# Kernel optimization log

Measured on AMD Instinct MI355X. Metric: run time of the kernel, lower is better.

## Reference

```python
import jax, jax.numpy as jnp
import numpy as np

D_MODEL, N_HEADS, D_HEAD = 1024, 16, 64
BATCH, SEQ = 4, 2048


def setup_inputs() -> dict:
    key = jax.random.key(0)
    ks = jax.random.split(key, 10)
    s = 1.0 / np.sqrt(D_MODEL)
    x = jax.random.normal(ks[0], (BATCH, SEQ, D_MODEL), dtype=jnp.float32)
    attention_mask = jax.random.randint(ks[1], (BATCH, SEQ), 0, 2).astype(jnp.bool_)
    # guarantee at least one attended key per batch row (avoid all -inf softmax)
    attention_mask = attention_mask.at[:, 0].set(True)
    def lin(k):
        kw, kb = jax.random.split(k)
        W = jax.random.uniform(kw, (D_MODEL, D_MODEL), jnp.float32, -s, s)
        b = jax.random.uniform(kb, (D_MODEL,), jnp.float32, -s, s)
        return W, b
    Wq, bq = lin(ks[2]); Wk, bk = lin(ks[3]); Wv, bv = lin(ks[4]); Wo, bo = lin(ks[5])
    return {"x": x, "attention_mask": attention_mask,
            "Wq": Wq, "bq": bq, "Wk": Wk, "bk": bk,
            "Wv": Wv, "bv": bv, "Wo": Wo, "bo": bo}


def reference(x, attention_mask, Wq, bq, Wk, bk, Wv, bv, Wo, bo):
    B, S, _ = x.shape
    def proj(W, b):  # [B,S,d_model] -> [B,S,H,Dh]
        return (x @ W + b).reshape(B, S, N_HEADS, D_HEAD)
    q = proj(Wq, bq)
    k = proj(Wk, bk)
    v = proj(Wv, bv)
    scores = jnp.einsum('bqhd,bkhd->bhqk', q, k)  # [B,H,S,S]
    add_mask = jnp.where(attention_mask, 0.0, jnp.inf)[:, None, None, :]
    # faithful order: subtract mask, THEN scale (inf survives division)
    probs = jax.nn.softmax((scores - add_mask) / jnp.sqrt(jnp.float32(D_HEAD)), axis=-1)
    attn = jnp.einsum('bhqk,bkhd->bqhd', probs, v).reshape(B, S, N_HEADS * D_HEAD)
    return attn @ Wo + bo
```

## Files before the change

### kernel.cpp

```cpp
#include <hip/hip_runtime.h>
#include <hip/hip_bf16.h>
#include <math.h>

#define BATCH 4
#define SEQ   2048
#define DM    1024
#define NH    16
#define DH    64
#define MROWS (BATCH * SEQ)

typedef unsigned short ushort_t;
typedef unsigned int   uint_t;
typedef __attribute__((ext_vector_type(8))) short  short8;
typedef __attribute__((ext_vector_type(4))) float  float4v;

#define QSCALE 0.1803368801111244f

__device__ __forceinline__ ushort_t f2bf(float v) {
    uint_t u = __float_as_uint(v);
    u += 0x7FFFu + ((u >> 16) & 1u);
    return (ushort_t)(u >> 16);
}
__device__ __forceinline__ float bf2f(ushort_t h) {
    return __uint_as_float(((uint_t)h) << 16);
}
__device__ __forceinline__ void gload_lds16(const ushort_t* g, ushort_t* lds) {
    __builtin_amdgcn_global_load_lds(
        (const __attribute__((address_space(1))) void*)g,
        (__attribute__((address_space(3))) void*)lds, 16, 0, 0);
}

__global__ __launch_bounds__(256) void conv_x(
    const float* __restrict__ src, ushort_t* __restrict__ dst, int n4)
{
    int i = blockIdx.x * 256 + threadIdx.x;
    if (i >= n4) return;
    float4 v = ((const float4*)src)[i];
    ((ushort4*)dst)[i] = make_ushort4(f2bf(v.x), f2bf(v.y), f2bf(v.z), f2bf(v.w));
}

__global__ __launch_bounds__(256) void convT_w4(
    const float* __restrict__ W0, const float* __restrict__ W1,
    const float* __restrict__ W2, const float* __restrict__ W3,
    ushort_t* __restrict__ fused, ushort_t* __restrict__ woh,
    ushort_t* __restrict__ wol)
{
    __shared__ float sT[64][65];
    const int z = blockIdx.z;
    const float* W = (z == 0) ? W0 : (z == 1) ? W1 : (z == 2) ? W2 : W3;
    ushort_t* ht = (z < 3) ? fused + (size_t)z * 1024 * 1024 : woh;
    const int n0 = blockIdx.x * 64, k0 = blockIdx.y * 64;
    const int t = threadIdx.x;
#pragma unroll
    for (int i = 0; i < 16; i++) {
        int idx = t + i * 256, r = idx >> 6, c = idx & 63;
        sT[r][c] = W[(size_t)(k0 + r) * 1024 + n0 + c];
    }
    __syncthreads();
#pragma unroll
    for (int i = 0; i < 16; i++) {
        int idx = t + i * 256, r = idx >> 6, c = idx & 63;
        float v = sT[c][r];
        ushort_t h = f2bf(v);
        ht[(size_t)(n0 + r) * 1024 + k0 + c] = h;
        if (z == 3) wol[(size_t)(n0 + r) * 1024 + k0 + c] = f2bf(v - bf2f(h));
    }
}

__global__ __launch_bounds__(256) void gemm_qkv(
    const ushort_t* __restrict__ A, const ushort_t* __restrict__ Bt,
    const float* __restrict__ bq, const float* __restrict__ bk,
    const float* __restrict__ bv,
    ushort_t* __restrict__ Qh, ushort_t* __restrict__ Kh,
    ushort_t* __restrict__ Vt)
{
    __shared__ __align__(16) ushort_t smem[8192];
    const int t = threadIdx.x, lane = t & 63, w = t >> 6;
    const int n0 = blockIdx.x * 128, m0 = blockIdx.y * 128;
    const int wm = (w >> 1) * 64, wn = (w & 1) * 64;
    const int lq = lane >> 4, lc = lane & 15;
    const int gl = (lane & 3) ^ ((lane >> 3) & 3);
    const int irow = lane >> 2;
    const int sect = n0 >> 10;
    const float* bsel = (sect == 0) ? bq : (sect == 1) ? bk : bv;
    const float scl = (sect == 0) ? QSCALE : 1.0f;

    float4v acc[4][4];
#pragma unroll
    for (int i = 0; i < 4; i++)
#pragma unroll
        for (int j = 0; j < 4; j++) acc[i][j] = (float4v)(0.0f);

    for (int k0 = 0; k0 < 1024; k0 += 32) {
        __syncthreads();
#pragma unroll
        for (int j = 0; j < 4; j++) {
            const int i = w * 4 + j;
            const ushort_t* src = (i < 8)
                ? A  + (size_t)(m0 + i * 16 + irow) * 1024 + k0 + gl * 8
                : Bt + (size_t)(n0 + (i - 8) * 16 + irow) * 1024 + k0 + gl * 8;
            gload_lds16(src, &smem[i * 512]);
        }
        __syncthreads();

        short8 av[4], bvf[4];
#pragma unroll
        for (int mt = 0; mt < 4; mt++) {
            const int r = wm + mt * 16 + lc;
            av[mt] = *(const short8*)&smem[r * 32 + ((lq ^ ((r >> 1) & 3)) * 8)];
        }
#pragma unroll
        for (int nt = 0; nt < 4; nt++) {
            const int r = wn + nt * 16 + lc;
            bvf[nt] = *(const short8*)&smem[4096 + r * 32 + ((lq ^ ((r >> 1) & 3)) * 8)];
        }
#pragma unroll
        for (int nt = 0; nt < 4; nt++)
#pragma unroll
            for (int mt = 0; mt < 4; mt++)
                acc[mt][nt] = __builtin_amdgcn_mfma_f32_16x16x32_bf16(av[mt], bvf[nt], acc[mt][nt], 0, 0, 0);
    }

#pragma unroll
    for (int nt = 0; nt < 4; nt++) {
        const int nn = (n0 + wn + nt * 16 + lc) & 1023;
        const float bvv = bsel[nn];
        const int h = nn >> 6, d = nn & 63;
#pragma unroll
        for (int mt = 0; mt < 4; mt++) {
            const int mbase = m0 + wm + mt * 16 + lq * 4;
            const int b = mbase >> 11, s0 = mbase & 2047;
            if (sect == 2) {
                ushort_t hh[4];
#pragma unroll
                for (int r = 0; r < 4; r++) hh[r] = f2bf(acc[mt][nt][r] + bvv);
                *(ushort4*)&Vt[((size_t)(b * 16 + h) * 64 + d) * 2048 + s0] =
                    make_ushort4(hh[0], hh[1], hh[2], hh[3]);
            } else {
                ushort_t* dst = (sect == 0) ? Qh : Kh;
#pragma unroll
                for (int r = 0; r < 4; r++)
                    dst[((size_t)(b * 16 + h) * 2048 + s0 + r) * 64 + d] =
                        f2bf((acc[mt][nt][r] + bvv) * scl);
            }
        }
    }
}

__global__ __launch_bounds__(256) void gemm_split3(
    const ushort_t* __restrict__ Ah, const ushort_t* __restrict__ Al,
    const ushort_t* __restrict__ Bh, const ushort_t* __restrict__ Bl,
    const float* __restrict__ bias, float* __restrict__ out)
{
    __shared__ __align__(16) ushort_t smem[16384];
    const int t = threadIdx.x, lane = t & 63, w = t >> 6;
    const int n0 = blockIdx.x * 128, m0 = blockIdx.y * 128;
    const int wm = (w >> 1) * 64, wn = (w & 1) * 64;
    const int lq = lane >> 4, lc = lane & 15;
    const int gl = (lane & 3) ^ ((lane >> 3) & 3);
    const int irow = lane >> 2;

    float4v acc[4][4];
#pragma unroll
    for (int i = 0; i < 4; i++)
#pragma unroll
        for (int j = 0; j < 4; j++) acc[i][j] = (float4v)(0.0f);

    const ushort_t* plane = (w == 0) ? Ah : (w == 1) ? Al : (w == 2) ? Bh : Bl;
    const size_t prow = (size_t)(((w < 2) ? m0 : n0) + irow) * 1024 + gl * 8;

    for (int k0 = 0; k0 < 1024; k0 += 32) {
        __syncthreads();
#pragma unroll
        for (int j = 0; j < 8; j++)
            gload_lds16(plane + prow + (size_t)j * 16384 + k0, &smem[w * 4096 + j * 512]);
        __syncthreads();

        short8 ah[4], al[4];
#pragma unroll
        for (int mt = 0; mt < 4; mt++) {
            const int r = wm + mt * 16 + lc;
            const int off = r * 32 + ((lq ^ ((r >> 1) & 3)) * 8);
            ah[mt] = *(const short8*)&smem[off];
            al[mt] = *(const short8*)&smem[4096 + off];
        }
#pragma unroll
        for (int nt = 0; nt < 4; nt++) {
            const int r = wn + nt * 16 + lc;
            const int off = r * 32 + ((lq ^ ((r >> 1) & 3)) * 8);
            short8 bh = *(const short8*)&smem[8192 + off];
            short8 bl = *(const short8*)&smem[12288 + off];
#pragma unroll
            for (int mt = 0; mt < 4; mt++) {
                acc[mt][nt] = __builtin_amdgcn_mfma_f32_16x16x32_bf16(ah[mt], bh, acc[mt][nt], 0, 0, 0);
                acc[mt][nt] = __builtin_amdgcn_mfma_f32_16x16x32_bf16(al[mt], bh, acc[mt][nt], 0, 0, 0);
                acc[mt][nt] = __builtin_amdgcn_mfma_f32_16x16x32_bf16(ah[mt], bl, acc[mt][nt], 0, 0, 0);
            }
        }
    }

#pragma unroll
    for (int nt = 0; nt < 4; nt++) {
        const int n = n0 + wn + nt * 16 + lc;
        const float bvv = bias[n];
#pragma unroll
        for (int mt = 0; mt < 4; mt++)
#pragma unroll
            for (int r = 0; r < 4; r++) {
                const int m = m0 + wm + mt * 16 + lq * 4 + r;
                out[(size_t)m * 1024 + n] = acc[mt][nt][r] + bvv;
            }
    }
}

__global__ __launch_bounds__(256, 4) void flash_mfma(
    const ushort_t* __restrict__ Q, const ushort_t* __restrict__ K,
    const ushort_t* __restrict__ Vt, const int* __restrict__ mask,
    ushort_t* __restrict__ Oh, ushort_t* __restrict__ Ol)
{
    __shared__ __align__(16) ushort_t smem[18432];
    const int t = threadIdx.x, lane = t & 63, w = t >> 6;
    const int q0 = blockIdx.x * 128;
    const int bh = blockIdx.y, b = bh >> 4, h = bh & 15;
    const int lq = lane >> 4, lc = lane & 15;
    const int wm = w * 32;
    const int gl = (lane & 7) ^ ((lane >> 3) & 7);

    const short8 onesf = (short8)(lc == 0 ? (short)0x3F80 : (short)0);

    {
        const ushort_t NEG = f2bf(-1e30f);
        const int4* mrow = (const int4*)(mask + b * SEQ);
        int4 a = mrow[t * 2], c = mrow[t * 2 + 1];
        ((ushort4*)&smem[16384])[t * 2] =
            make_ushort4(a.x ? 0 : NEG, a.y ? 0 : NEG, a.z ? 0 : NEG, a.w ? 0 : NEG);
        ((ushort4*)&smem[16384])[t * 2 + 1] =
            make_ushort4(c.x ? 0 : NEG, c.y ? 0 : NEG, c.z ? 0 : NEG, c.w ? 0 : NEG);
    }
#pragma unroll
    for (int j = 0; j < 4; j++) {
        const int i = w * 4 + j;
        gload_lds16(Q + ((size_t)bh * SEQ + q0 + i * 8 + (lane >> 3)) * 64 + gl * 8,
                    &smem[i * 512]);
    }
    __syncthreads();

    short8 aq[2][2];
#pragma unroll
    for (int mt = 0; mt < 2; mt++)
#pragma unroll
        for (int kk = 0; kk < 2; kk++) {
            const int r = wm + mt * 16 + lc;
            aq[mt][kk] = *(const short8*)&smem[r * 64 + (((kk * 4 + lq) ^ (r & 7)) * 8)];
        }

    float4v O[2][4];
    float4v lacc[2];
#pragma unroll
    for (int mt = 0; mt < 2; mt++) {
#pragma unroll
        for (int nt = 0; nt < 4; nt++) O[mt][nt] = (float4v)(0.0f);
        lacc[mt] = (float4v)(0.0f);
    }

    for (int kt = 0; kt < 32; kt++) {
        const int k0 = kt * 64;
        __syncthreads();
#pragma unroll
        for (int j = 0; j < 4; j++) {
            const int i = w * 4 + j;
            if (i < 8)
                gload_lds16(K + ((size_t)bh * SEQ + k0 + i * 8 + (lane >> 3)) * 64 + gl * 8,
                            &smem[8192 + i * 512]);
            else
                gload_lds16(Vt + ((size_t)bh * 64 + (i - 8) * 8 + (lane >> 3)) * SEQ + k0 + gl * 8,
                            &smem[12288 + (i - 8) * 512]);
        }
        __syncthreads();

        float4v binit[4];
#pragma unroll
        for (int kt4 = 0; kt4 < 4; kt4++) {
            const ushort4 bb = *(const ushort4*)&smem[16384 + k0 + kt4 * 16 + lq * 4];
            binit[kt4][0] = bf2f(bb.x); binit[kt4][1] = bf2f(bb.y);
            binit[kt4][2] = bf2f(bb.z); binit[kt4][3] = bf2f(bb.w);
        }

        float4v sc[4][2];
#pragma unroll
        for (int kt4 = 0; kt4 < 4; kt4++)
#pragma unroll
            for (int mt = 0; mt < 2; mt++) sc[kt4][mt] = binit[kt4];
#pragma unroll
        for (int kk = 0; kk < 2; kk++) {
#pragma unroll
            for (int kt4 = 0; kt4 < 4; kt4++) {
                const int kr = kt4 * 16 + lc;
                short8 ak = *(const short8*)&smem[8192 + kr * 64 + (((kk * 4 + lq) ^ (kr & 7)) * 8)];
#pragma unroll
                for (int mt = 0; mt < 2; mt++)
                    sc[kt4][mt] = __builtin_amdgcn_mfma_f32_16x16x32_bf16(ak, aq[mt][kk], sc[kt4][mt], 0, 0, 0);
            }
        }

#pragma unroll
        for (int kt4 = 0; kt4 < 4; kt4++) {
#pragma unroll
            for (int mt = 0; mt < 2; mt++) {
                const int qr = wm + mt * 16 + lc;
                const float p0 = __builtin_amdgcn_exp2f(sc[kt4][mt][0]);
                const float p1 = __builtin_amdgcn_exp2f(sc[kt4][mt][1]);
                const float p2 = __builtin_amdgcn_exp2f(sc[kt4][mt][2]);
                const float p3 = __builtin_amdgcn_exp2f(sc[kt4][mt][3]);
                __hip_bfloat162 pk01 = __float22bfloat162_rn(make_float2(p0, p1));
                __hip_bfloat162 pk23 = __float22bfloat162_rn(make_float2(p2, p3));
                *(uint2*)&smem[qr * 64 + (((kt4 * 2 + (lq >> 1)) ^ (qr & 7)) * 8) + (lq & 1) * 4] =
                    make_uint2(*(const uint_t*)&pk01, *(const uint_t*)&pk23);
            }
        }

#pragma unroll
        for (int kk = 0; kk < 2; kk++) {
            short8 ap[2];
#pragma unroll
            for (int mt = 0; mt < 2; mt++) {
                const int qr = wm + mt * 16 + lc;
                ap[mt] = *(const short8*)&smem[qr * 64 + (((kk * 4 + lq) ^ (qr & 7)) * 8)];
            }
#pragma unroll
            for (int mt = 0; mt < 2; mt++)
                lacc[mt] = __builtin_amdgcn_mfma_f32_16x16x32_bf16(ap[mt], onesf, lacc[mt], 0, 0, 0);
#pragma unroll
            for (int nt = 0; nt < 4; nt++) {
                const int d = nt * 16 + lc;
                short8 bv = *(const short8*)&smem[12288 + d * 64 + (((kk * 4 + lq) ^ (d & 7)) * 8)];
#pragma unroll
                for (int mt = 0; mt < 2; mt++)
                    O[mt][nt] = __builtin_amdgcn_mfma_f32_16x16x32_bf16(ap[mt], bv, O[mt][nt], 0, 0, 0);
            }
        }
    }

#pragma unroll
    for (int mt = 0; mt < 2; mt++) {
#pragma unroll
        for (int r = 0; r < 4; r++) {
            const float lsum = __shfl(lacc[mt][r], lane & 48);
            const float inv = 1.0f / lsum;
            const int srow = q0 + wm + mt * 16 + lq * 4 + r;
#pragma unroll
            for (int nt = 0; nt < 4; nt++) {
                const float v = O[mt][nt][r] * inv;
                const ushort_t hh = f2bf(v);
                const size_t idx = ((size_t)(b * SEQ + srow)) * 1024 + h * 64 + nt * 16 + lc;
                Oh[idx] = hh;
                Ol[idx] = f2bf(v - bf2f(hh));
            }
        }
    }
}

extern "C" void kernel_launch(void* const* d_in, const int* in_sizes, int n_in,
                              void* d_out, int out_size, void* d_ws, size_t ws_size,
                              hipStream_t stream) {
    const float* x    = (const float*)d_in[0];
    const int*   mask = (const int*)d_in[1];
    const float* Wq   = (const float*)d_in[2];
    const float* bq   = (const float*)d_in[3];
    const float* Wk   = (const float*)d_in[4];
    const float* bk   = (const float*)d_in[5];
    const float* Wv   = (const float*)d_in[6];
    const float* bv   = (const float*)d_in[7];
    const float* Wo   = (const float*)d_in[8];
    const float* bo   = (const float*)d_in[9];
    float* out = (float*)d_out;

    ushort_t* p = (ushort_t*)d_ws;
    const size_t PLANE  = (size_t)MROWS * DM;
    const size_t WPLANE = (size_t)DM * DM;
    ushort_t* xh  = p;  p += PLANE;
    ushort_t* wf  = p;  p += 3 * WPLANE;
    ushort_t* woh = p;  p += WPLANE;
    ushort_t* wol = p;  p += WPLANE;
    ushort_t* Qh  = p;  p += PLANE;
    ushort_t* Kh  = p;  p += PLANE;
    ushort_t* Vth = p;  p += PLANE;
    ushort_t* Ath = p;  p += PLANE;
    ushort_t* Atl = p;  p += PLANE;

    dim3 blk(256);
    hipLaunchKernelGGL(conv_x, dim3(8192), blk, 0, stream, x, xh, 2097152);
    hipLaunchKernelGGL(convT_w4, dim3(16, 16, 4), blk, 0, stream,
                       Wq, Wk, Wv, Wo, wf, woh, wol);
    hipLaunchKernelGGL(gemm_qkv, dim3(24, 64), blk, 0, stream,
                       xh, wf, bq, bk, bv, Qh, Kh, Vth);
    hipLaunchKernelGGL(flash_mfma, dim3(16, 64), blk, 0, stream,
                       Qh, Kh, Vth, mask, Ath, Atl);
    hipLaunchKernelGGL(gemm_split3, dim3(8, 64), blk, 0, stream,
                       Ath, Atl, woh, wol, bo, out);
}
```

Measured before the change: 326.0 us.

## Fold key mask into K/V projection and correct softmax denominator by masked count

The QKV GEMM epilogue now zeroes K and V rows at masked key positions. Each masked score then becomes exactly 0, giving exp2(0)=1 in the row sum, and the flash kernel subtracts the per-batch masked-key count from the denominator. This removes the per-tile mask-bias load and bf16-to-float conversion from the attention inner loop and shrinks LDS usage. Alongside that, LDS and global addresses are precomputed outside the loop so the tile loads use one strided pointer per wave. The denominator subtraction runs in fp32 against a sum of bf16-rounded probabilities, so cancellation error can appear when most keys are masked.

```diff
diff --git a/kernel.cpp b/kernel.cpp
--- a/kernel.cpp
+++ b/kernel.cpp
@@ -70,7 +70,7 @@
 __global__ __launch_bounds__(256) void gemm_qkv(
     const ushort_t* __restrict__ A, const ushort_t* __restrict__ Bt,
     const float* __restrict__ bq, const float* __restrict__ bk,
-    const float* __restrict__ bv,
+    const float* __restrict__ bv, const int* __restrict__ mask,
     ushort_t* __restrict__ Qh, ushort_t* __restrict__ Kh,
     ushort_t* __restrict__ Vt)
 {
@@ -130,10 +130,16 @@
         for (int mt = 0; mt < 4; mt++) {
             const int mbase = m0 + wm + mt * 16 + lq * 4;
             const int b = mbase >> 11, s0 = mbase & 2047;
+            int mk[4] = {1, 1, 1, 1};
+            if (sect != 0) {
+                const int4 m4 = *(const int4*)&mask[b * 2048 + s0];
+                mk[0] = m4.x; mk[1] = m4.y; mk[2] = m4.z; mk[3] = m4.w;
+            }
             if (sect == 2) {
                 ushort_t hh[4];
 #pragma unroll
-                for (int r = 0; r < 4; r++) hh[r] = f2bf(acc[mt][nt][r] + bvv);
+                for (int r = 0; r < 4; r++)
+                    hh[r] = mk[r] ? f2bf(acc[mt][nt][r] + bvv) : (ushort_t)0;
                 *(ushort4*)&Vt[((size_t)(b * 16 + h) * 64 + d) * 2048 + s0] =
                     make_ushort4(hh[0], hh[1], hh[2], hh[3]);
             } else {
@@ -141,7 +147,7 @@
 #pragma unroll
                 for (int r = 0; r < 4; r++)
                     dst[((size_t)(b * 16 + h) * 2048 + s0 + r) * 64 + d] =
-                        f2bf((acc[mt][nt][r] + bvv) * scl);
+                        mk[r] ? f2bf((acc[mt][nt][r] + bvv) * scl) : (ushort_t)0;
             }
         }
     }
@@ -218,24 +224,26 @@
     const ushort_t* __restrict__ Vt, const int* __restrict__ mask,
     ushort_t* __restrict__ Oh, ushort_t* __restrict__ Ol)
 {
-    __shared__ __align__(16) ushort_t smem[18432];
+    __shared__ __align__(16) ushort_t smem[16384];
     const int t = threadIdx.x, lane = t & 63, w = t >> 6;
     const int q0 = blockIdx.x * 128;
     const int bh = blockIdx.y, b = bh >> 4, h = bh & 15;
     const int lq = lane >> 4, lc = lane & 15;
     const int wm = w * 32;
     const int gl = (lane & 7) ^ ((lane >> 3) & 7);
+    const int lc7 = lc & 7;
 
     const short8 onesf = (short8)(lc == 0 ? (short)0x3F80 : (short)0);
 
+    int cnt;
     {
-        const ushort_t NEG = f2bf(-1e30f);
         const int4* mrow = (const int4*)(mask + b * SEQ);
-        int4 a = mrow[t * 2], c = mrow[t * 2 + 1];
-        ((ushort4*)&smem[16384])[t * 2] =
-            make_ushort4(a.x ? 0 : NEG, a.y ? 0 : NEG, a.z ? 0 : NEG, a.w ? 0 : NEG);
-        ((ushort4*)&smem[16384])[t * 2 + 1] =
-            make_ushort4(c.x ? 0 : NEG, c.y ? 0 : NEG, c.z ? 0 : NEG, c.w ? 0 : NEG);
+        const int4 a = mrow[t * 2], c = mrow[t * 2 + 1];
+        cnt = (a.x == 0) + (a.y == 0) + (a.z == 0) + (a.w == 0) +
+              (c.x == 0) + (c.y == 0) + (c.z == 0) + (c.w == 0);
+#pragma unroll
+        for (int off = 1; off < 64; off <<= 1) cnt += __shfl_xor(cnt, off);
+        if (lane == 0) ((float*)&smem[8192])[w] = (float)cnt;
     }
 #pragma unroll
     for (int j = 0; j < 4; j++) {
@@ -244,6 +252,8 @@
                     &smem[i * 512]);
     }
     __syncthreads();
+    const float nmaskf = ((const float*)&smem[8192])[0] + ((const float*)&smem[8192])[1] +
+                         ((const float*)&smem[8192])[2] + ((const float*)&smem[8192])[3];
 
     short8 aq[2][2];
 #pragma unroll
@@ -254,6 +264,28 @@
             aq[mt][kk] = *(const short8*)&smem[r * 64 + (((kk * 4 + lq) ^ (r & 7)) * 8)];
         }
 
+    int aK[2], aPw[4], aPr[2];
+#pragma unroll
+    for (int kk = 0; kk < 2; kk++) {
+        aK[kk]  = lc * 64 + (((kk * 4 + lq) ^ lc7) * 8);
+        aPr[kk] = wm * 64 + aK[kk];
+    }
+#pragma unroll
+    for (int kt4 = 0; kt4 < 4; kt4++)
+        aPw[kt4] = wm * 64 + lc * 64 + (((kt4 * 2 + (lq >> 1)) ^ lc7) * 8) + (lq & 1) * 4;
+
+    const ushort_t* gsrc;
+    int gstride;
+    int dstbase;
+    int jstride;
+    if (w < 2) {
+        gsrc = K + ((size_t)bh * SEQ + w * 32 + (lane >> 3)) * 64 + gl * 8;
+        gstride = 64 * 64;  dstbase = 8192 + w * 2048;  jstride = 512;
+    } else {
+        gsrc = Vt + ((size_t)bh * 64 + (w - 2) * 32 + (lane >> 3)) * SEQ + gl * 8;
+        gstride = 64;       dstbase = 12288 + (w - 2) * 2048;  jstride = 8 * 2048;
+    }
+
     float4v O[2][4];
     float4v lacc[2];
 #pragma unroll
@@ -264,39 +296,23 @@
     }
 
     for (int kt = 0; kt < 32; kt++) {
-        const int k0 = kt * 64;
-        __syncthreads();
-#pragma unroll
-        for (int j = 0; j < 4; j++) {
-            const int i = w * 4 + j;
-            if (i < 8)
-                gload_lds16(K + ((size_t)bh * SEQ + k0 + i * 8 + (lane >> 3)) * 64 + gl * 8,
-                            &smem[8192 + i * 512]);
-            else
-                gload_lds16(Vt + ((size_t)bh * 64 + (i - 8) * 8 + (lane >> 3)) * SEQ + k0 + gl * 8,
-                            &smem[12288 + (i - 8) * 512]);
-        }
-        __syncthreads();
-
-        float4v binit[4];
-#pragma unroll
-        for (int kt4 = 0; kt4 < 4; kt4++) {
-            const ushort4 bb = *(const ushort4*)&smem[16384 + k0 + kt4 * 16 + lq * 4];
-            binit[kt4][0] = bf2f(bb.x); binit[kt4][1] = bf2f(bb.y);
-            binit[kt4][2] = bf2f(bb.z); binit[kt4][3] = bf2f(bb.w);
-        }
+        __syncthreads();
+#pragma unroll
+        for (int j = 0; j < 4; j++)
+            gload_lds16(gsrc + j * jstride, &smem[dstbase + j * 512]);
+        gsrc += gstride;
+        __syncthreads();
 
         float4v sc[4][2];
 #pragma unroll
         for (int kt4 = 0; kt4 < 4; kt4++)
 #pragma unroll
-            for (int mt = 0; mt < 2; mt++) sc[kt4][mt] = binit[kt4];
+            for (int mt = 0; mt < 2; mt++) sc[kt4][mt] = (float4v)(0.0f);
 #pragma unroll
         for (int kk = 0; kk < 2; kk++) {
 #pragma unroll
             for (int kt4 = 0; kt4 < 4; kt4++) {
-                const int kr = kt4 * 16 + lc;
-                short8 ak = *(const short8*)&smem[8192 + kr * 64 + (((kk * 4 + lq) ^ (kr & 7)) * 8)];
+                short8 ak = *(const short8*)&smem[8192 + kt4 * 1024 + aK[kk]];
 #pragma unroll
                 for (int mt = 0; mt < 2; mt++)
                     sc[kt4][mt] = __builtin_amdgcn_mfma_f32_16x16x32_bf16(ak, aq[mt][kk], sc[kt4][mt], 0, 0, 0);
@@ -307,14 +323,13 @@
         for (int kt4 = 0; kt4 < 4; kt4++) {
 #pragma unroll
             for (int mt = 0; mt < 2; mt++) {
-                const int qr = wm + mt * 16 + lc;
                 const float p0 = __builtin_amdgcn_exp2f(sc[kt4][mt][0]);
                 const float p1 = __builtin_amdgcn_exp2f(sc[kt4][mt][1]);
                 const float p2 = __builtin_amdgcn_exp2f(sc[kt4][mt][2]);
                 const float p3 = __builtin_amdgcn_exp2f(sc[kt4][mt][3]);
                 __hip_bfloat162 pk01 = __float22bfloat162_rn(make_float2(p0, p1));
                 __hip_bfloat162 pk23 = __float22bfloat162_rn(make_float2(p2, p3));
-                *(uint2*)&smem[qr * 64 + (((kt4 * 2 + (lq >> 1)) ^ (qr & 7)) * 8) + (lq & 1) * 4] =
+                *(uint2*)&smem[mt * 1024 + aPw[kt4]] =
                     make_uint2(*(const uint_t*)&pk01, *(const uint_t*)&pk23);
             }
         }
@@ -323,17 +338,14 @@
         for (int kk = 0; kk < 2; kk++) {
             short8 ap[2];
 #pragma unroll
-            for (int mt = 0; mt < 2; mt++) {
-                const int qr = wm + mt * 16 + lc;
-                ap[mt] = *(const short8*)&smem[qr * 64 + (((kk * 4 + lq) ^ (qr & 7)) * 8)];
-            }
+            for (int mt = 0; mt < 2; mt++)
+                ap[mt] = *(const short8*)&smem[mt * 1024 + aPr[kk]];
 #pragma unroll
             for (int mt = 0; mt < 2; mt++)
                 lacc[mt] = __builtin_amdgcn_mfma_f32_16x16x32_bf16(ap[mt], onesf, lacc[mt], 0, 0, 0);
 #pragma unroll
             for (int nt = 0; nt < 4; nt++) {
-                const int d = nt * 16 + lc;
-                short8 bv = *(const short8*)&smem[12288 + d * 64 + (((kk * 4 + lq) ^ (d & 7)) * 8)];
+                short8 bv = *(const short8*)&smem[12288 + nt * 1024 + aK[kk]];
 #pragma unroll
                 for (int mt = 0; mt < 2; mt++)
                     O[mt][nt] = __builtin_amdgcn_mfma_f32_16x16x32_bf16(ap[mt], bv, O[mt][nt], 0, 0, 0);
@@ -345,7 +357,7 @@
     for (int mt = 0; mt < 2; mt++) {
 #pragma unroll
         for (int r = 0; r < 4; r++) {
-            const float lsum = __shfl(lacc[mt][r], lane & 48);
+            const float lsum = __shfl(lacc[mt][r], lane & 48) - nmaskf;
             const float inv = 1.0f / lsum;
             const int srow = q0 + wm + mt * 16 + lq * 4 + r;
 #pragma unroll
@@ -393,7 +405,7 @@
     hipLaunchKernelGGL(convT_w4, dim3(16, 16, 4), blk, 0, stream,
                        Wq, Wk, Wv, Wo, wf, woh, wol);
     hipLaunchKernelGGL(gemm_qkv, dim3(24, 64), blk, 0, stream,
-                       xh, wf, bq, bk, bv, Qh, Kh, Vth);
+                       xh, wf, bq, bk, bv, mask, Qh, Kh, Vth);
     hipLaunchKernelGGL(flash_mfma, dim3(16, 64), blk, 0, stream,
                        Qh, Kh, Vth, mask, Ath, Atl);
     hipLaunchKernelGGL(gemm_split3, dim3(8, 64), blk, 0, stream,
```

Result: faster. 311.8 us (-4.3%).
